# Optimization experiments

Measured on AMD Instinct MI355X. Metric: run time of the kernel, lower is better.

## Reference

```python
import jax, jax.numpy as jnp
import numpy as np

HEADS, HDIM, GROUPS, EPS = 8, 64, 8, 1e-5

def setup_inputs() -> dict:
    key = jax.random.key(0)
    ks = jax.random.split(key, 3)
    c, inner = 256, HEADS * HDIM
    return {
        "x": jax.random.normal(ks[0], (2, c, 16, 16, 16), dtype=jnp.float32),
        "gamma": jnp.ones((c,), jnp.float32),
        "beta": jnp.zeros((c,), jnp.float32),
        "w_qkv": jax.random.normal(ks[1], (3 * inner, c), dtype=jnp.float32) * (c ** -0.5),
        "b_qkv": jnp.zeros((3 * inner,), jnp.float32),
        "w_out": jax.random.normal(ks[2], (c, inner), dtype=jnp.float32) * (inner ** -0.5),
        "b_out": jnp.zeros((c,), jnp.float32),
    }

def reference(x, gamma, beta, w_qkv, b_qkv, w_out, b_out):
    b, c, d, h, w = x.shape
    n = d * h * w
    scale = HDIM ** -0.5
    # GroupNorm(8, c)
    xg = x.reshape(b, GROUPS, c // GROUPS, d, h, w)
    mu = xg.mean(axis=(2, 3, 4, 5), keepdims=True)
    var = xg.var(axis=(2, 3, 4, 5), keepdims=True)
    xn = ((xg - mu) * jax.lax.rsqrt(var + EPS)).reshape(b, c, d, h, w)
    xn = xn * gamma[None, :, None, None, None] + beta[None, :, None, None, None]
    # 1x1x1 conv -> qkv, channel order (three, heads, dim)
    qkv = jnp.einsum('oc,bcdhw->bodhw', w_qkv, xn) + b_qkv[None, :, None, None, None]
    qkv = qkv.reshape(b, 3, HEADS, HDIM, n).transpose(1, 0, 2, 4, 3)  # [3,b,heads,n,dim]
    q, k, v = qkv[0], qkv[1], qkv[2]
    attn = jax.nn.softmax(jnp.einsum('bhnd,bhmd->bhnm', q, k) * scale, axis=-1)
    out = jnp.einsum('bhnm,bhmd->bhnd', attn, v)  # [b,heads,n,dim]
    out = out.transpose(0, 1, 3, 2).reshape(b, HEADS * HDIM, d, h, w)  # (heads dim) channels
    y = jnp.einsum('oc,bcdhw->bodhw', w_out, out) + b_out[None, :, None, None, None]
    # Dropout(0.1) in eval mode = identity
    return y + x
```

## Files before the change

kernel.cpp:

```cpp
#include <hip/hip_runtime.h>
#include <hip/hip_bf16.h>


typedef __attribute__((ext_vector_type(8))) short bf8_t;
typedef __attribute__((ext_vector_type(4))) float f4_t;

#define NTOK 4096
#define GRP_ELEMS (32 * 4096)

__device__ __forceinline__ unsigned short f2bf(float f) {
  union { float f; unsigned int i; } v; v.f = f;
  unsigned int r = v.i + 0x7fffu + ((v.i >> 16) & 1u);
  return (unsigned short)(r >> 16);
}

__device__ __forceinline__ unsigned int pkbf(float a, float b) {
  float2 t; t.x = a; t.y = b;
  __hip_bfloat162 h = __float22bfloat162_rn(t);
  union { __hip_bfloat162 h; unsigned int u; } c; c.h = h;
  return c.u;
}

__device__ __forceinline__ void gl_lds16(const unsigned short* g, unsigned short* l) {
  __builtin_amdgcn_global_load_lds((const __attribute__((address_space(1))) void*)g,
                                   (__attribute__((address_space(3))) void*)l, 16, 0, 0);
}

__device__ __forceinline__ bf8_t ldsw128(const unsigned short* base, int row, int du) {
  return *(const bf8_t*)((const char*)base + (((row << 7) + (du << 4)) ^ ((row & 7) << 4)));
}
__device__ __forceinline__ bf8_t ldsw64(const unsigned short* base, int row, int du) {
  return *(const bf8_t*)((const char*)base + (((row << 6) + (du << 4)) ^ (((row >> 1) & 3) << 4)));
}

#if __has_builtin(__builtin_amdgcn_exp2f)
#define EXP2 __builtin_amdgcn_exp2f
#else
#define EXP2 exp2f
#endif

__global__ __launch_bounds__(256) void gn_stats(const float* __restrict__ x, float* __restrict__ stats) {
  int g = blockIdx.y, sp = blockIdx.x;
  const float4* p = (const float4*)(x + (size_t)g * GRP_ELEMS + (size_t)sp * 8192);
  float s = 0.f, s2 = 0.f;
  for (int i = threadIdx.x; i < 2048; i += 256) {
    float4 v = p[i];
    s  += v.x + v.y + v.z + v.w;
    s2 += v.x * v.x + v.y * v.y + v.z * v.z + v.w * v.w;
  }
  for (int m = 32; m; m >>= 1) { s += __shfl_xor(s, m); s2 += __shfl_xor(s2, m); }
  __shared__ float rs[4][2];
  int wv = threadIdx.x >> 6;
  if ((threadIdx.x & 63) == 0) { rs[wv][0] = s; rs[wv][1] = s2; }
  __syncthreads();
  if (threadIdx.x == 0) {
    float ts = rs[0][0] + rs[1][0] + rs[2][0] + rs[3][0];
    float t2 = rs[0][1] + rs[1][1] + rs[2][1] + rs[3][1];
    atomicAdd(&stats[g], ts);
    atomicAdd(&stats[16 + g], t2);
  }
}

__global__ __launch_bounds__(256) void gn_apply(const float* __restrict__ x,
    const float* __restrict__ gamma, const float* __restrict__ beta,
    const float* __restrict__ stats, unsigned short* __restrict__ xnt) {
  __shared__ float t[64][65];
  int b = blockIdx.z, c0 = blockIdx.y * 64, n0 = blockIdx.x * 64;
  int tr = threadIdx.x >> 2;
  int tc = (threadIdx.x & 3) * 16;
  int c = c0 + tr;
  int g = b * 8 + (c >> 5);
  float mu = stats[g] * (1.f / GRP_ELEMS);
  float var = stats[16 + g] * (1.f / GRP_ELEMS) - mu * mu;
  float rstd = rsqrtf(var + 1e-5f);
  float sc = gamma[c] * rstd;
  float sh = beta[c] - mu * sc;
  const float* xp = x + ((size_t)(b * 256 + c)) * NTOK + n0 + tc;
  for (int q = 0; q < 4; ++q) {
    float4 v = *(const float4*)(xp + q * 4);
    t[tr][tc + q * 4 + 0] = v.x * sc + sh;
    t[tr][tc + q * 4 + 1] = v.y * sc + sh;
    t[tr][tc + q * 4 + 2] = v.z * sc + sh;
    t[tr][tc + q * 4 + 3] = v.w * sc + sh;
  }
  __syncthreads();
  int n = n0 + tr;
  union { unsigned short s[16]; uint4 u[2]; } tmp;
  for (int q = 0; q < 16; ++q) tmp.s[q] = f2bf(t[tc + q][tr]);
  uint4* dst = (uint4*)(xnt + ((size_t)b * NTOK + n) * 256 + c0 + tc);
  dst[0] = tmp.u[0];
  dst[1] = tmp.u[1];
}

__global__ __launch_bounds__(256) void cast_w(const float* __restrict__ wqkv, const float* __restrict__ wout,
    unsigned short* __restrict__ wq, unsigned short* __restrict__ wo) {
  int i = blockIdx.x * 256 + threadIdx.x;
  const float* src; unsigned short* dst; int off;
  if (i < 98304) { src = wqkv; dst = wq; off = i; }
  else           { src = wout; dst = wo; off = i - 98304; }
  float4 v = ((const float4*)src)[off];
  union { unsigned short s[4]; uint2 u; } o;
  o.s[0] = f2bf(v.x); o.s[1] = f2bf(v.y); o.s[2] = f2bf(v.z); o.s[3] = f2bf(v.w);
  *(uint2*)(dst + (size_t)off * 4) = o.u;
}

__global__ __launch_bounds__(256) void qkv_gemm(const unsigned short* __restrict__ wq,
    const unsigned short* __restrict__ xnt, const float* __restrict__ bqkv,
    unsigned short* __restrict__ Qg, unsigned short* __restrict__ Kg, unsigned short* __restrict__ Vt) {
  __shared__ unsigned short Al[2][4096];
  __shared__ unsigned short Bl[2][4096];
  int b = blockIdx.z, m0 = blockIdx.y * 128, n0 = blockIdx.x * 128;
  const unsigned short* Ap = wq + (size_t)m0 * 256;
  const unsigned short* Bp = xnt + ((size_t)b * NTOK + n0) * 256;
  int lane = threadIdx.x & 63, wv = threadIdx.x >> 6;
  int lq = lane & 15, hq = lane >> 4;
  int m_off = (wv >> 1) * 64, n_off = (wv & 1) * 64;
  f4_t acc[4][4] = {};
  {
    for (int is = 0; is < 2; ++is) {
      int ck = wv * 128 + is * 64 + lane;
      int r = ck >> 2, cu = ck & 3;
      int csw = (cu ^ ((r >> 1) & 3)) << 3;
      gl_lds16(Ap + (size_t)r * 256 + csw, &Al[0][(wv * 128 + is * 64) * 8]);
      gl_lds16(Bp + (size_t)r * 256 + csw, &Bl[0][(wv * 128 + is * 64) * 8]);
    }
  }
  __syncthreads();
  for (int kt = 0; kt < 8; ++kt) {
    int cb = kt & 1, nb = cb ^ 1;
    if (kt < 7) {
      int k0 = (kt + 1) * 32;
      for (int is = 0; is < 2; ++is) {
        int ck = wv * 128 + is * 64 + lane;
        int r = ck >> 2, cu = ck & 3;
        int csw = (cu ^ ((r >> 1) & 3)) << 3;
        gl_lds16(Ap + (size_t)r * 256 + k0 + csw, &Al[nb][(wv * 128 + is * 64) * 8]);
        gl_lds16(Bp + (size_t)r * 256 + k0 + csw, &Bl[nb][(wv * 128 + is * 64) * 8]);
      }
    }
    const unsigned short* Ac = Al[cb];
    const unsigned short* Bc = Bl[cb];
    bf8_t af[4], bfr[4];
    for (int i = 0; i < 4; ++i) af[i]  = ldsw64(Ac, m_off + i * 16 + lq, hq);
    for (int j = 0; j < 4; ++j) bfr[j] = ldsw64(Bc, n_off + j * 16 + lq, hq);
    for (int i = 0; i < 4; ++i)
      for (int j = 0; j < 4; ++j)
        acc[i][j] = __builtin_amdgcn_mfma_f32_16x16x32_bf16(af[i], bfr[j], acc[i][j], 0, 0, 0);
    __syncthreads();
  }
  int tq = m0 >> 9;
  if (tq < 2) {
    unsigned short* dst = tq == 0 ? Qg : Kg;
    float sc = tq == 0 ? 0.1803368801111243f : 1.0f;
    for (int i = 0; i < 4; ++i)
      for (int j = 0; j < 4; ++j) {
        int o0 = m0 + m_off + i * 16 + hq * 4;
        int n = n0 + n_off + j * 16 + lq;
        int h = (o0 >> 6) & 7, dd0 = o0 & 63;
        size_t bh = (size_t)b * 8 + h;
        uint2 pk;
        pk.x = pkbf((acc[i][j][0] + bqkv[o0 + 0]) * sc, (acc[i][j][1] + bqkv[o0 + 1]) * sc);
        pk.y = pkbf((acc[i][j][2] + bqkv[o0 + 2]) * sc, (acc[i][j][3] + bqkv[o0 + 3]) * sc);
        *(uint2*)(dst + (bh * NTOK + n) * 64 + dd0) = pk;
      }
  } else {
    for (int i = 0; i < 4; ++i)
      for (int j = 0; j < 4; ++j) {
        int n = n0 + n_off + j * 16 + lq;
        for (int jj = 0; jj < 4; ++jj) {
          int o = m0 + m_off + i * 16 + hq * 4 + jj;
          int h = (o >> 6) & 7, dd = o & 63;
          size_t bh = (size_t)b * 8 + h;
          Vt[(bh * 64 + dd) * NTOK + n] = f2bf(acc[i][j][jj] + bqkv[o]);
        }
      }
  }
}

__global__ __launch_bounds__(256) void attn(const unsigned short* __restrict__ Qg,
    const unsigned short* __restrict__ Kg, const unsigned short* __restrict__ Vt,
    unsigned short* __restrict__ att) {
  __shared__ unsigned short Kls[2][4096];
  __shared__ unsigned short Vls[2][4096];
  __shared__ unsigned short Pls[4][1024];
  int bid = blockIdx.x;
  int bh = (bid & 7) * 2 + (bid >> 9);
  int q0 = ((bid >> 3) & 63) * 64;
  int b = bh >> 3, h = bh & 7;
  const unsigned short* kp = Kg + (size_t)bh * NTOK * 64;
  const unsigned short* vp = Vt + (size_t)bh * 64 * NTOK;
  int lane = threadIdx.x & 63, wv = threadIdx.x >> 6;
  int lq = lane & 15, hq = lane >> 4;
  unsigned short* Pw = &Pls[wv][0];
  const unsigned short* qp = Qg + ((size_t)bh * NTOK + q0 + wv * 16) * 64;
  bf8_t aq[2];
  for (int ks = 0; ks < 2; ++ks)
    aq[ks] = *(const bf8_t*)(qp + (size_t)lq * 64 + ks * 32 + hq * 8);
  f4_t accO[4] = {};
  float ls = 0.f;
  {
    for (int is = 0; is < 2; ++is) {
      int ck = wv * 128 + is * 64 + lane;
      int r = ck >> 3, cu = ck & 7;
      int csw = (cu ^ (r & 7)) << 3;
      gl_lds16(kp + (size_t)r * 64 + csw, &Kls[0][ck * 8]);
      gl_lds16(vp + (size_t)r * NTOK + csw, &Vls[0][ck * 8]);
    }
  }
  __syncthreads();
  #pragma unroll 2
  for (int t = 0; t < 64; ++t) {
    int cb = t & 1, nb = cb ^ 1;
    if (t < 63) {
      int tn = t + 1;
      for (int is = 0; is < 2; ++is) {
        int ck = wv * 128 + is * 64 + lane;
        int r = ck >> 3, cu = ck & 7;
        int csw = (cu ^ (r & 7)) << 3;
        gl_lds16(kp + (size_t)(tn * 64 + r) * 64 + csw, &Kls[nb][ck * 8]);
        gl_lds16(vp + (size_t)r * NTOK + tn * 64 + csw, &Vls[nb][ck * 8]);
      }
    }
    const unsigned short* Kc = Kls[cb];
    const unsigned short* Vc = Vls[cb];
    f4_t s[4] = {};
    for (int ks = 0; ks < 2; ++ks)
      for (int kvf = 0; kvf < 4; ++kvf) {
        bf8_t ak = ldsw128(Kc, kvf * 16 + lq, ks * 4 + hq);
        s[kvf] = __builtin_amdgcn_mfma_f32_16x16x32_bf16(ak, aq[ks], s[kvf], 0, 0, 0);
      }
    float rs = 0.f;
    for (int kvf = 0; kvf < 4; ++kvf)
      for (int jj = 0; jj < 4; ++jj) {
        float p = EXP2(s[kvf][jj]);
        s[kvf][jj] = p;
        rs += p;
      }
    ls += rs;
    for (int kvf = 0; kvf < 4; ++kvf) {
      uint2 pk;
      pk.x = pkbf(s[kvf][0], s[kvf][1]);
      pk.y = pkbf(s[kvf][2], s[kvf][3]);
      *(uint2*)((char*)Pw + (((lq << 7) + kvf * 32 + hq * 8) ^ ((lq & 7) << 4))) = pk;
    }
    for (int ks = 0; ks < 2; ++ks) {
      bf8_t pb = ldsw128(Pw, lq, ks * 4 + hq);
      for (int df = 0; df < 4; ++df) {
        bf8_t av = ldsw128(Vc, df * 16 + lq, ks * 4 + hq);
        accO[df] = __builtin_amdgcn_mfma_f32_16x16x32_bf16(av, pb, accO[df], 0, 0, 0);
      }
    }
    __syncthreads();
  }
  ls += __shfl_xor(ls, 16);
  ls += __shfl_xor(ls, 32);
  float inv = 1.0f / ls;
  int q = q0 + wv * 16 + lq;
  unsigned short* op = att + ((size_t)b * NTOK + q) * 512 + h * 64;
  for (int df = 0; df < 4; ++df) {
    int d0 = df * 16 + hq * 4;
    uint2 pk;
    pk.x = pkbf(accO[df][0] * inv, accO[df][1] * inv);
    pk.y = pkbf(accO[df][2] * inv, accO[df][3] * inv);
    *(uint2*)(op + d0) = pk;
  }
}

__global__ __launch_bounds__(256) void out_proj(const unsigned short* __restrict__ wo,
    const unsigned short* __restrict__ att, const float* __restrict__ bout,
    const float* __restrict__ x, float* __restrict__ y) {
  __shared__ unsigned short Al[2][2048];
  __shared__ unsigned short Bl[2][4096];
  int b = blockIdx.z, m0 = blockIdx.y * 64, n0 = blockIdx.x * 128;
  const unsigned short* Ap = wo + (size_t)m0 * 512;
  const unsigned short* Bp = att + ((size_t)b * NTOK + n0) * 512;
  int lane = threadIdx.x & 63, wv = threadIdx.x >> 6;
  int lq = lane & 15, hq = lane >> 4;
  int m_off = (wv >> 1) * 32, n_off = (wv & 1) * 64;
  f4_t acc[2][4] = {};
  {
    int ckA = wv * 64 + lane;
    int rA = ckA >> 2, cuA = ckA & 3;
    gl_lds16(Ap + (size_t)rA * 512 + ((cuA ^ ((rA >> 1) & 3)) << 3), &Al[0][(wv * 64) * 8]);
    for (int is = 0; is < 2; ++is) {
      int ck = wv * 128 + is * 64 + lane;
      int r = ck >> 2, cu = ck & 3;
      gl_lds16(Bp + (size_t)r * 512 + ((cu ^ ((r >> 1) & 3)) << 3), &Bl[0][(wv * 128 + is * 64) * 8]);
    }
  }
  __syncthreads();
  for (int kt = 0; kt < 16; ++kt) {
    int cb = kt & 1, nb = cb ^ 1;
    if (kt < 15) {
      int k0 = (kt + 1) * 32;
      int ckA = wv * 64 + lane;
      int rA = ckA >> 2, cuA = ckA & 3;
      gl_lds16(Ap + (size_t)rA * 512 + k0 + ((cuA ^ ((rA >> 1) & 3)) << 3), &Al[nb][(wv * 64) * 8]);
      for (int is = 0; is < 2; ++is) {
        int ck = wv * 128 + is * 64 + lane;
        int r = ck >> 2, cu = ck & 3;
        gl_lds16(Bp + (size_t)r * 512 + k0 + ((cu ^ ((r >> 1) & 3)) << 3), &Bl[nb][(wv * 128 + is * 64) * 8]);
      }
    }
    const unsigned short* Ac = Al[cb];
    const unsigned short* Bc = Bl[cb];
    bf8_t af[2], bfr[4];
    for (int i = 0; i < 2; ++i) af[i]  = ldsw64(Ac, m_off + i * 16 + lq, hq);
    for (int j = 0; j < 4; ++j) bfr[j] = ldsw64(Bc, n_off + j * 16 + lq, hq);
    for (int i = 0; i < 2; ++i)
      for (int j = 0; j < 4; ++j)
        acc[i][j] = __builtin_amdgcn_mfma_f32_16x16x32_bf16(af[i], bfr[j], acc[i][j], 0, 0, 0);
    __syncthreads();
  }
  for (int i = 0; i < 2; ++i)
    for (int j = 0; j < 4; ++j) {
      int n = n0 + n_off + j * 16 + lq;
      for (int jj = 0; jj < 4; ++jj) {
        int co = m0 + m_off + i * 16 + hq * 4 + jj;
        size_t idx = ((size_t)b * 256 + co) * NTOK + n;
        y[idx] = acc[i][j][jj] + bout[co] + x[idx];
      }
    }
}

extern "C" void kernel_launch(void* const* d_in, const int* in_sizes, int n_in,
                              void* d_out, int out_size, void* d_ws, size_t ws_size,
                              hipStream_t stream) {
  const float* x     = (const float*)d_in[0];
  const float* gamma = (const float*)d_in[1];
  const float* beta  = (const float*)d_in[2];
  const float* wqkv  = (const float*)d_in[3];
  const float* bqkv  = (const float*)d_in[4];
  const float* wout  = (const float*)d_in[5];
  const float* bout  = (const float*)d_in[6];
  float* y = (float*)d_out;

  char* ws = (char*)d_ws;
  float*          stats = (float*)ws;
  unsigned short* WQ    = (unsigned short*)(ws + 256);
  unsigned short* WO    = (unsigned short*)(ws + 786688);
  unsigned short* XNT   = (unsigned short*)(ws + 1048832);
  unsigned short* Qg    = (unsigned short*)(ws + 5243136);
  unsigned short* Kg    = (unsigned short*)(ws + 13631744);
  unsigned short* Vt    = (unsigned short*)(ws + 22020352);
  unsigned short* ATT   = (unsigned short*)(ws + 30408960);

  hipMemsetAsync(stats, 0, 128, stream);
  gn_stats<<<dim3(16, 16), 256, 0, stream>>>(x, stats);
  gn_apply<<<dim3(64, 4, 2), 256, 0, stream>>>(x, gamma, beta, stats, XNT);
  cast_w<<<512, 256, 0, stream>>>(wqkv, wout, WQ, WO);
  qkv_gemm<<<dim3(32, 12, 2), 256, 0, stream>>>(WQ, XNT, bqkv, Qg, Kg, Vt);
  attn<<<1024, 256, 0, stream>>>(Qg, Kg, Vt, ATT);
  out_proj<<<dim3(32, 4, 2), 256, 0, stream>>>(WO, ATT, bout, x, y);
}
```

Baseline: 217.4 us.

## Use 32x32 MFMA in attention with register-shuffled P and merge weight cast

The attention kernel switches from 16x16x32 to 32x32x16 bf16 MFMA, with 2 waves of 32 query rows each instead of 4 waves of 16. The P tile is now passed between the two MFMAs through a cross-half lane shuffle rather than an LDS round trip, and the MFMA sections are wrapped in s_setprio. Separately, the weight-cast kernel is merged into the GroupNorm stats kernel to save one launch. The cost is fewer waves per block and more accumulator registers per lane, which may lower occupancy or latency hiding.

```diff
diff --git a/kernel.cpp b/kernel.cpp
--- a/kernel.cpp
+++ b/kernel.cpp
@@ -4,6 +4,7 @@
 
 typedef __attribute__((ext_vector_type(8))) short bf8_t;
 typedef __attribute__((ext_vector_type(4))) float f4_t;
+typedef __attribute__((ext_vector_type(16))) float f16v;
 
 #define NTOK 4096
 #define GRP_ELEMS (32 * 4096)
@@ -39,8 +40,22 @@
 #define EXP2 exp2f
 #endif
 
-__global__ __launch_bounds__(256) void gn_stats(const float* __restrict__ x, float* __restrict__ stats) {
-  int g = blockIdx.y, sp = blockIdx.x;
+__global__ __launch_bounds__(256) void gn_stats_castw(const float* __restrict__ x, float* __restrict__ stats,
+    const float* __restrict__ wqkv, const float* __restrict__ wout,
+    unsigned short* __restrict__ wq, unsigned short* __restrict__ wo) {
+  int bid = blockIdx.x;
+  if (bid >= 256) {
+    int i = (bid - 256) * 256 + threadIdx.x;
+    const float* src; unsigned short* dst; int off;
+    if (i < 98304) { src = wqkv; dst = wq; off = i; }
+    else           { src = wout; dst = wo; off = i - 98304; }
+    float4 v = ((const float4*)src)[off];
+    union { unsigned short s[4]; uint2 u; } o;
+    o.s[0] = f2bf(v.x); o.s[1] = f2bf(v.y); o.s[2] = f2bf(v.z); o.s[3] = f2bf(v.w);
+    *(uint2*)(dst + (size_t)off * 4) = o.u;
+    return;
+  }
+  int g = bid & 15, sp = bid >> 4;
   const float4* p = (const float4*)(x + (size_t)g * GRP_ELEMS + (size_t)sp * 8192);
   float s = 0.f, s2 = 0.f;
   for (int i = threadIdx.x; i < 2048; i += 256) {
@@ -92,18 +107,6 @@
   dst[1] = tmp.u[1];
 }
 
-__global__ __launch_bounds__(256) void cast_w(const float* __restrict__ wqkv, const float* __restrict__ wout,
-    unsigned short* __restrict__ wq, unsigned short* __restrict__ wo) {
-  int i = blockIdx.x * 256 + threadIdx.x;
-  const float* src; unsigned short* dst; int off;
-  if (i < 98304) { src = wqkv; dst = wq; off = i; }
-  else           { src = wout; dst = wo; off = i - 98304; }
-  float4 v = ((const float4*)src)[off];
-  union { unsigned short s[4]; uint2 u; } o;
-  o.s[0] = f2bf(v.x); o.s[1] = f2bf(v.y); o.s[2] = f2bf(v.z); o.s[3] = f2bf(v.w);
-  *(uint2*)(dst + (size_t)off * 4) = o.u;
-}
-
 __global__ __launch_bounds__(256) void qkv_gemm(const unsigned short* __restrict__ wq,
     const unsigned short* __restrict__ xnt, const float* __restrict__ bqkv,
     unsigned short* __restrict__ Qg, unsigned short* __restrict__ Kg, unsigned short* __restrict__ Vt) {
@@ -177,30 +180,29 @@
   }
 }
 
-__global__ __launch_bounds__(256) void attn(const unsigned short* __restrict__ Qg,
+__global__ __launch_bounds__(128) void attn(const unsigned short* __restrict__ Qg,
     const unsigned short* __restrict__ Kg, const unsigned short* __restrict__ Vt,
     unsigned short* __restrict__ att) {
   __shared__ unsigned short Kls[2][4096];
   __shared__ unsigned short Vls[2][4096];
-  __shared__ unsigned short Pls[4][1024];
   int bid = blockIdx.x;
   int bh = (bid & 7) * 2 + (bid >> 9);
   int q0 = ((bid >> 3) & 63) * 64;
   int b = bh >> 3, h = bh & 7;
   const unsigned short* kp = Kg + (size_t)bh * NTOK * 64;
   const unsigned short* vp = Vt + (size_t)bh * 64 * NTOK;
-  int lane = threadIdx.x & 63, wv = threadIdx.x >> 6;
-  int lq = lane & 15, hq = lane >> 4;
-  unsigned short* Pw = &Pls[wv][0];
-  const unsigned short* qp = Qg + ((size_t)bh * NTOK + q0 + wv * 16) * 64;
-  bf8_t aq[2];
-  for (int ks = 0; ks < 2; ++ks)
-    aq[ks] = *(const bf8_t*)(qp + (size_t)lq * 64 + ks * 32 + hq * 8);
-  f4_t accO[4] = {};
+  int tid = threadIdx.x;
+  int lane = tid & 63, wv = tid >> 6;
+  int l31 = lane & 31, h5 = lane >> 5;
+  const unsigned short* qp = Qg + ((size_t)bh * NTOK + q0 + wv * 32 + l31) * 64;
+  bf8_t aq[4];
+  for (int t4 = 0; t4 < 4; ++t4)
+    aq[t4] = *(const bf8_t*)(qp + t4 * 16 + h5 * 8);
+  f16v accO[2] = {};
   float ls = 0.f;
   {
-    for (int is = 0; is < 2; ++is) {
-      int ck = wv * 128 + is * 64 + lane;
+    for (int is = 0; is < 4; ++is) {
+      int ck = is * 128 + tid;
       int r = ck >> 3, cu = ck & 7;
       int csw = (cu ^ (r & 7)) << 3;
       gl_lds16(kp + (size_t)r * 64 + csw, &Kls[0][ck * 8]);
@@ -213,8 +215,8 @@
     int cb = t & 1, nb = cb ^ 1;
     if (t < 63) {
       int tn = t + 1;
-      for (int is = 0; is < 2; ++is) {
-        int ck = wv * 128 + is * 64 + lane;
+      for (int is = 0; is < 4; ++is) {
+        int ck = is * 128 + tid;
         int r = ck >> 3, cu = ck & 7;
         int csw = (cu ^ (r & 7)) << 3;
         gl_lds16(kp + (size_t)(tn * 64 + r) * 64 + csw, &Kls[nb][ck * 8]);
@@ -223,47 +225,69 @@
     }
     const unsigned short* Kc = Kls[cb];
     const unsigned short* Vc = Vls[cb];
-    f4_t s[4] = {};
-    for (int ks = 0; ks < 2; ++ks)
-      for (int kvf = 0; kvf < 4; ++kvf) {
-        bf8_t ak = ldsw128(Kc, kvf * 16 + lq, ks * 4 + hq);
-        s[kvf] = __builtin_amdgcn_mfma_f32_16x16x32_bf16(ak, aq[ks], s[kvf], 0, 0, 0);
-      }
+    f16v s[2] = {};
+    __builtin_amdgcn_s_setprio(1);
+    #pragma unroll
+    for (int t4 = 0; t4 < 4; ++t4) {
+      bf8_t ak0 = ldsw128(Kc, l31, 2 * t4 + h5);
+      bf8_t ak1 = ldsw128(Kc, 32 + l31, 2 * t4 + h5);
+      s[0] = __builtin_amdgcn_mfma_f32_32x32x16_bf16(ak0, aq[t4], s[0], 0, 0, 0);
+      s[1] = __builtin_amdgcn_mfma_f32_32x32x16_bf16(ak1, aq[t4], s[1], 0, 0, 0);
+    }
+    __builtin_amdgcn_s_setprio(0);
     float rs = 0.f;
-    for (int kvf = 0; kvf < 4; ++kvf)
-      for (int jj = 0; jj < 4; ++jj) {
-        float p = EXP2(s[kvf][jj]);
-        s[kvf][jj] = p;
+    #pragma unroll
+    for (int kvb = 0; kvb < 2; ++kvb)
+      #pragma unroll
+      for (int r = 0; r < 16; ++r) {
+        float p = EXP2(s[kvb][r]);
+        s[kvb][r] = p;
         rs += p;
       }
     ls += rs;
-    for (int kvf = 0; kvf < 4; ++kvf) {
-      uint2 pk;
-      pk.x = pkbf(s[kvf][0], s[kvf][1]);
-      pk.y = pkbf(s[kvf][2], s[kvf][3]);
-      *(uint2*)((char*)Pw + (((lq << 7) + kvf * 32 + hq * 8) ^ ((lq & 7) << 4))) = pk;
-    }
-    for (int ks = 0; ks < 2; ++ks) {
-      bf8_t pb = ldsw128(Pw, lq, ks * 4 + hq);
-      for (int df = 0; df < 4; ++df) {
-        bf8_t av = ldsw128(Vc, df * 16 + lq, ks * 4 + hq);
-        accO[df] = __builtin_amdgcn_mfma_f32_16x16x32_bf16(av, pb, accO[df], 0, 0, 0);
-      }
-    }
+    bf8_t pb[4];
+    #pragma unroll
+    for (int t4 = 0; t4 < 4; ++t4) {
+      int kvb = t4 >> 1, r0 = (t4 & 1) * 8;
+      unsigned int pA0 = pkbf(s[kvb][r0 + 0], s[kvb][r0 + 1]);
+      unsigned int pA1 = pkbf(s[kvb][r0 + 2], s[kvb][r0 + 3]);
+      unsigned int pB0 = pkbf(s[kvb][r0 + 4], s[kvb][r0 + 5]);
+      unsigned int pB1 = pkbf(s[kvb][r0 + 6], s[kvb][r0 + 7]);
+      unsigned int send0 = h5 ? pA0 : pB0;
+      unsigned int send1 = h5 ? pA1 : pB1;
+      unsigned int recv0 = __shfl_xor(send0, 32);
+      unsigned int recv1 = __shfl_xor(send1, 32);
+      union { unsigned int u[4]; bf8_t v; } pk;
+      pk.u[0] = h5 ? recv0 : pA0;
+      pk.u[1] = h5 ? recv1 : pA1;
+      pk.u[2] = h5 ? pB0 : recv0;
+      pk.u[3] = h5 ? pB1 : recv1;
+      pb[t4] = pk.v;
+    }
+    __builtin_amdgcn_s_setprio(1);
+    #pragma unroll
+    for (int t4 = 0; t4 < 4; ++t4) {
+      bf8_t av0 = ldsw128(Vc, l31, 2 * t4 + h5);
+      bf8_t av1 = ldsw128(Vc, 32 + l31, 2 * t4 + h5);
+      accO[0] = __builtin_amdgcn_mfma_f32_32x32x16_bf16(av0, pb[t4], accO[0], 0, 0, 0);
+      accO[1] = __builtin_amdgcn_mfma_f32_32x32x16_bf16(av1, pb[t4], accO[1], 0, 0, 0);
+    }
+    __builtin_amdgcn_s_setprio(0);
     __syncthreads();
   }
-  ls += __shfl_xor(ls, 16);
   ls += __shfl_xor(ls, 32);
   float inv = 1.0f / ls;
-  int q = q0 + wv * 16 + lq;
+  int q = q0 + wv * 32 + l31;
   unsigned short* op = att + ((size_t)b * NTOK + q) * 512 + h * 64;
-  for (int df = 0; df < 4; ++df) {
-    int d0 = df * 16 + hq * 4;
-    uint2 pk;
-    pk.x = pkbf(accO[df][0] * inv, accO[df][1] * inv);
-    pk.y = pkbf(accO[df][2] * inv, accO[df][3] * inv);
-    *(uint2*)(op + d0) = pk;
-  }
+  #pragma unroll
+  for (int db = 0; db < 2; ++db)
+    #pragma unroll
+    for (int g = 0; g < 4; ++g) {
+      uint2 pk;
+      pk.x = pkbf(accO[db][g * 4 + 0] * inv, accO[db][g * 4 + 1] * inv);
+      pk.y = pkbf(accO[db][g * 4 + 2] * inv, accO[db][g * 4 + 3] * inv);
+      *(uint2*)(op + db * 32 + g * 8 + h5 * 4) = pk;
+    }
 }
 
 __global__ __launch_bounds__(256) void out_proj(const unsigned short* __restrict__ wo,
@@ -346,10 +370,9 @@
   unsigned short* ATT   = (unsigned short*)(ws + 30408960);
 
   hipMemsetAsync(stats, 0, 128, stream);
-  gn_stats<<<dim3(16, 16), 256, 0, stream>>>(x, stats);
+  gn_stats_castw<<<768, 256, 0, stream>>>(x, stats, wqkv, wout, WQ, WO);
   gn_apply<<<dim3(64, 4, 2), 256, 0, stream>>>(x, gamma, beta, stats, XNT);
-  cast_w<<<512, 256, 0, stream>>>(wqkv, wout, WQ, WO);
   qkv_gemm<<<dim3(32, 12, 2), 256, 0, stream>>>(WQ, XNT, bqkv, Qg, Kg, Vt);
-  attn<<<1024, 256, 0, stream>>>(Qg, Kg, Vt, ATT);
+  attn<<<1024, 128, 0, stream>>>(Qg, Kg, Vt, ATT);
   out_proj<<<dim3(32, 4, 2), 256, 0, stream>>>(WO, ATT, bout, x, y);
 }
```

Measured after the change: 219.7 us. No clear change (+1.1%).
